# Kernel tuning notes

Hardware: AMD Instinct MI355X
Metric: run time of the kernel (lower is better)

The kernel has to match this reference:

```python
import jax, jax.numpy as jnp
import numpy as np

B, S, D, H = 4, 2048, 1024, 16


def setup_inputs() -> dict:
    key = jax.random.key(0)
    ks = jax.random.split(key, 9)
    scale = 0.02  # keep logits in a sane range
    x = jax.random.normal(ks[0], (B, S, D), dtype=jnp.float32)
    Wq = jax.random.normal(ks[1], (D, D), dtype=jnp.float32) * scale
    bq = jax.random.normal(ks[2], (D,), dtype=jnp.float32) * scale
    Wk = jax.random.normal(ks[3], (D, D), dtype=jnp.float32) * scale
    bk = jax.random.normal(ks[4], (D,), dtype=jnp.float32) * scale
    Wv = jax.random.normal(ks[5], (D, D), dtype=jnp.float32) * scale
    bv = jax.random.normal(ks[6], (D,), dtype=jnp.float32) * scale
    Wo = jax.random.normal(ks[7], (D, D), dtype=jnp.float32) * scale
    bo = jax.random.normal(ks[8], (D,), dtype=jnp.float32) * scale
    return {"x": x, "Wq": Wq, "bq": bq, "Wk": Wk, "bk": bk,
            "Wv": Wv, "bv": bv, "Wo": Wo, "bo": bo}


def _apply_rope(x):
    """Rotate-half RoPE over the full feature dim (applied pre-projection)."""
    b, s, d = x.shape
    half = d // 2
    # theta_i = 10000^(-2i/d), i in [0, d/2)
    freq = jnp.exp(jnp.arange(0, d, 2, dtype=jnp.float32) * (-np.log(10000.0) / d))
    ang = jnp.arange(s, dtype=jnp.float32)[:, None] * freq[None, :]  # [S, d/2]
    cos, sin = jnp.cos(ang), jnp.sin(ang)
    x1, x2 = x[..., :half], x[..., half:]
    return jnp.concatenate([x1 * cos - x2 * sin, x1 * sin + x2 * cos], axis=-1)


def reference(x, Wq, bq, Wk, bk, Wv, bv, Wo, bo):
    b, s, d = x.shape
    h = H
    hd = d // h
    rx = _apply_rope(x)  # [B, S, D]

    def proj(W, bias):
        y = rx @ W.T + bias                       # torch Linear: x W^T + b
        return y.reshape(b, s, h, hd).transpose(0, 2, 1, 3)  # [B, H, S, hd]

    q, k, v = proj(Wq, bq), proj(Wk, bk), proj(Wv, bv)
    scores = jnp.einsum('bhqd,bhkd->bhqk', q, k) / np.sqrt(hd)
    attn = jax.nn.softmax(scores, axis=-1)
    attended = jnp.einsum('bhqk,bhkd->bhqd', attn, v)
    attended = attended.transpose(0, 2, 1, 3).reshape(b, s, d)
    return attended @ Wo.T + bo
```

## Files before the change

kernel.cpp:

```cpp
#include <hip/hip_runtime.h>

#define NB 4
#define NS 2048
#define ND 1024
#define NH 16
#define HD 64

using bf16x8 = __attribute__((ext_vector_type(8))) short;
using f32x4  = __attribute__((ext_vector_type(4))) float;

__device__ __forceinline__ unsigned short f2bf(float f) {
  union { float f; unsigned u; } a; a.f = f;
  unsigned r = a.u + 0x7FFF + ((a.u >> 16) & 1);
  return (unsigned short)(r >> 16);
}

__device__ __forceinline__ void gload_lds16(const void* g, void* l) {
  __builtin_amdgcn_global_load_lds(
      (const __attribute__((address_space(1))) void*)g,
      (__attribute__((address_space(3))) void*)l, 16, 0, 0);
}

__global__ __launch_bounds__(256) void rope_kernel(const float* __restrict__ x,
                                                   unsigned short* __restrict__ rx) {
  int idx = blockIdx.x * 256 + threadIdx.x;
  int j  = idx & 511;
  int bs = idx >> 9;
  int s  = bs & (NS - 1);
  const float* xp = x + (size_t)bs * ND;
  float ang = (float)s * __expf((float)j * -0.017988946039f);
  float sn, cs;
  __sincosf(ang, &sn, &cs);
  float x1 = xp[j], x2 = xp[j + 512];
  unsigned short* rp = rx + (size_t)bs * ND;
  rp[j]       = f2bf(x1 * cs - x2 * sn);
  rp[j + 512] = f2bf(x1 * sn + x2 * cs);
}

__global__ __launch_bounds__(256) void wconv_kernel(const float* __restrict__ w0,
                                                    const float* __restrict__ w1,
                                                    const float* __restrict__ w2,
                                                    const float* __restrict__ w3,
                                                    unsigned short* __restrict__ wb) {
  int idx = blockIdx.x * 256 + threadIdx.x;
  int e = idx << 2;
  const float* w = (e < (1 << 20)) ? w0 : (e < (2 << 20)) ? w1 : (e < (3 << 20)) ? w2 : w3;
  float4 v = *(const float4*)(w + (e & 0xFFFFF));
  ushort4 o;
  o.x = f2bf(v.x); o.y = f2bf(v.y); o.z = f2bf(v.z); o.w = f2bf(v.w);
  *(ushort4*)(wb + e) = o;
}

__global__ __launch_bounds__(256) void gemm_qkv(const unsigned short* __restrict__ A,
                                                const unsigned short* __restrict__ Wb,
                                                const float* __restrict__ bq,
                                                const float* __restrict__ bk,
                                                const float* __restrict__ bv,
                                                unsigned short* __restrict__ q,
                                                unsigned short* __restrict__ k,
                                                unsigned short* __restrict__ vt) {
  __shared__ alignas(16) unsigned short As[128 * 32];
  __shared__ alignas(16) unsigned short Bs[128 * 32];
  const int tid = threadIdx.x;
  const int lane = tid & 63;
  const int wid = tid >> 6;
  const int wm = wid >> 1, wn = wid & 1;
  const int l15 = lane & 15, lg = lane >> 4;
  const int m0 = blockIdx.x * 128;
  const int n0 = blockIdx.y * 128;
  const int z = blockIdx.z;
  const unsigned short* Bp = Wb + ((size_t)z << 20);

  f32x4 acc[4][4] = {};

  for (int k0 = 0; k0 < ND; k0 += 32) {
#pragma unroll
    for (int it = 0; it < 2; ++it) {
      int c = it * 256 + tid;
      int row = c >> 2, kc = (c & 3) << 3;
      int ldsbase = (it * 256 + (tid & 192)) << 3;
      gload_lds16(A  + (size_t)(m0 + row) * ND + k0 + kc, As + ldsbase);
      gload_lds16(Bp + (size_t)(n0 + row) * ND + k0 + kc, Bs + ldsbase);
    }
    __syncthreads();
    bf16x8 af[4], bfr[4];
#pragma unroll
    for (int m = 0; m < 4; ++m)
      af[m] = *(const bf16x8*)(As + (wm * 64 + m * 16 + l15) * 32 + lg * 8);
#pragma unroll
    for (int n = 0; n < 4; ++n)
      bfr[n] = *(const bf16x8*)(Bs + (wn * 64 + n * 16 + l15) * 32 + lg * 8);
#pragma unroll
    for (int m = 0; m < 4; ++m)
#pragma unroll
      for (int n = 0; n < 4; ++n)
        acc[m][n] = __builtin_amdgcn_mfma_f32_16x16x32_bf16(af[m], bfr[n], acc[m][n], 0, 0, 0);
    __syncthreads();
  }

  const float* bias = (z == 0) ? bq : (z == 1) ? bk : bv;
#pragma unroll
  for (int n = 0; n < 4; ++n) {
    int col = n0 + wn * 64 + n * 16 + l15;
    float bb = bias[col];
    int hh = col >> 6, dd = col & 63;
#pragma unroll
    for (int m = 0; m < 4; ++m) {
#pragma unroll
      for (int r = 0; r < 4; ++r) {
        int rowi = m0 + wm * 64 + m * 16 + lg * 4 + r;
        int bbi = rowi >> 11, ss = rowi & (NS - 1);
        unsigned short val = f2bf(acc[m][n][r] + bb);
        size_t bhoff = (size_t)(bbi * NH + hh);
        if (z == 0)      q [(bhoff * NS + ss) * HD + dd] = val;
        else if (z == 1) k [(bhoff * NS + ss) * HD + dd] = val;
        else             vt[(bhoff * HD + dd) * NS + ss] = val;
      }
    }
  }
}

__global__ __launch_bounds__(256) void attn_kernel(const unsigned short* __restrict__ q,
                                                   const unsigned short* __restrict__ k,
                                                   const unsigned short* __restrict__ vt,
                                                   unsigned short* __restrict__ att) {
  __shared__ alignas(16) unsigned short Ks[2][64 * 64];
  __shared__ alignas(16) unsigned short Vs[2][64 * 64];
  __shared__ alignas(16) unsigned short Ps[4][32 * 64];
  const int tid = threadIdx.x;
  const int lane = tid & 63;
  const int w = tid >> 6;
  const int l15 = lane & 15, lg = lane >> 4;

  const int id = blockIdx.x;
  const int swz = (id & 7) * 128 + (id >> 3);
  const int bh = swz >> 4;
  const int b = bh >> 4, h = bh & 15;
  const int q0 = (swz & 15) * 128;

  const unsigned short* qp = q  + (size_t)bh * NS * HD;
  const unsigned short* kp = k  + (size_t)bh * NS * HD;
  const unsigned short* vp = vt + (size_t)bh * HD * NS;

  bf16x8 qf[2][2];
#pragma unroll
  for (int m = 0; m < 2; ++m)
#pragma unroll
    for (int t = 0; t < 2; ++t)
      qf[m][t] = *(const bf16x8*)(qp + (size_t)(q0 + w * 32 + m * 16 + l15) * HD + t * 32 + lg * 8);

  f32x4 o[2][4] = {};
  float run_m[2][4], run_l[2][4];
#pragma unroll
  for (int m = 0; m < 2; ++m)
#pragma unroll
    for (int r = 0; r < 4; ++r) { run_m[m][r] = -1e30f; run_l[m][r] = 0.f; }

  unsigned short* ps = &Ps[w][0];

  const int c0 = tid;
#define STAGE(buf, t0)                                                          \
  {                                                                             \
    _Pragma("unroll")                                                           \
    for (int it = 0; it < 2; ++it) {                                            \
      int c = it * 256 + c0;                                                    \
      int ro = c >> 3;                                                          \
      int chs = (c & 7) ^ (ro & 7);                                             \
      int ldsbase = (it * 256 + (tid & 192)) << 3;                              \
      gload_lds16(kp + (size_t)((t0) + ro) * HD + (chs << 3), Ks[buf] + ldsbase); \
      gload_lds16(vp + (size_t)ro * NS + (t0) + (chs << 3),   Vs[buf] + ldsbase); \
    }                                                                           \
  }

  STAGE(0, 0);
  __syncthreads();
  int cur = 0;

  for (int t0 = 0; t0 < NS; t0 += 64) {
    if (t0 + 64 < NS) STAGE(cur ^ 1, t0 + 64);

    f32x4 sc[2][4] = {};
#pragma unroll
    for (int kk = 0; kk < 2; ++kk)
#pragma unroll
      for (int n = 0; n < 4; ++n) {
        int krow = n * 16 + l15;
        bf16x8 kf = *(const bf16x8*)(Ks[cur] + krow * 64 + (((kk * 4 + lg) ^ (krow & 7)) << 3));
#pragma unroll
        for (int m = 0; m < 2; ++m)
          sc[m][n] = __builtin_amdgcn_mfma_f32_16x16x32_bf16(qf[m][kk], kf, sc[m][n], 0, 0, 0);
      }

#pragma unroll
    for (int m = 0; m < 2; ++m)
#pragma unroll
      for (int r = 0; r < 4; ++r) {
        float mx = fmaxf(fmaxf(sc[m][0][r], sc[m][1][r]), fmaxf(sc[m][2][r], sc[m][3][r]));
        mx = fmaxf(mx, __shfl_xor(mx, 1));
        mx = fmaxf(mx, __shfl_xor(mx, 2));
        mx = fmaxf(mx, __shfl_xor(mx, 4));
        mx = fmaxf(mx, __shfl_xor(mx, 8));
        float nm = fmaxf(run_m[m][r], mx);
        float fac = __expf(0.125f * (run_m[m][r] - nm));
        run_m[m][r] = nm;
        float rs = 0.f;
#pragma unroll
        for (int n = 0; n < 4; ++n) {
          float p = __expf(0.125f * (sc[m][n][r] - nm));
          sc[m][n][r] = p;
          rs += p;
        }
        rs += __shfl_xor(rs, 1);
        rs += __shfl_xor(rs, 2);
        rs += __shfl_xor(rs, 4);
        rs += __shfl_xor(rs, 8);
        run_l[m][r] = run_l[m][r] * fac + rs;
#pragma unroll
        for (int n = 0; n < 4; ++n) o[m][n][r] *= fac;
      }

#pragma unroll
    for (int m = 0; m < 2; ++m)
#pragma unroll
      for (int n = 0; n < 4; ++n)
#pragma unroll
        for (int r = 0; r < 4; ++r) {
          int prow = m * 16 + lg * 4 + r;
          ps[prow * 64 + ((n * 16 + l15) ^ ((prow & 7) << 3))] = f2bf(sc[m][n][r]);
        }

    bf16x8 pf[2][2];
#pragma unroll
    for (int m = 0; m < 2; ++m)
#pragma unroll
      for (int kk = 0; kk < 2; ++kk)
        pf[m][kk] = *(const bf16x8*)(ps + (m * 16 + l15) * 64 + (((kk * 4 + lg) ^ (l15 & 7)) << 3));

#pragma unroll
    for (int kk = 0; kk < 2; ++kk)
#pragma unroll
      for (int n = 0; n < 4; ++n) {
        int vrow = n * 16 + l15;
        bf16x8 vf = *(const bf16x8*)(Vs[cur] + vrow * 64 + (((kk * 4 + lg) ^ (vrow & 7)) << 3));
#pragma unroll
        for (int m = 0; m < 2; ++m)
          o[m][n] = __builtin_amdgcn_mfma_f32_16x16x32_bf16(pf[m][kk], vf, o[m][n], 0, 0, 0);
      }
    __syncthreads();
    cur ^= 1;
  }
#undef STAGE

#pragma unroll
  for (int m = 0; m < 2; ++m)
#pragma unroll
    for (int r = 0; r < 4; ++r) {
      int rowi = q0 + w * 32 + m * 16 + lg * 4 + r;
      float inv = 1.0f / run_l[m][r];
#pragma unroll
      for (int n = 0; n < 4; ++n)
        att[((size_t)(b * NS + rowi)) * ND + h * HD + n * 16 + l15] = f2bf(o[m][n][r] * inv);
    }
}

__global__ __launch_bounds__(256) void gemm_out(const unsigned short* __restrict__ A,
                                                const unsigned short* __restrict__ Bw,
                                                const float* __restrict__ bo,
                                                float* __restrict__ out) {
  __shared__ alignas(16) unsigned short As[128 * 32];
  __shared__ alignas(16) unsigned short Bs[128 * 32];
  const int tid = threadIdx.x;
  const int lane = tid & 63;
  const int wid = tid >> 6;
  const int wm = wid >> 1, wn = wid & 1;
  const int l15 = lane & 15, lg = lane >> 4;
  const int m0 = blockIdx.x * 128;
  const int n0 = blockIdx.y * 128;

  f32x4 acc[4][4] = {};

  for (int k0 = 0; k0 < ND; k0 += 32) {
#pragma unroll
    for (int it = 0; it < 2; ++it) {
      int c = it * 256 + tid;
      int row = c >> 2, kc = (c & 3) << 3;
      int ldsbase = (it * 256 + (tid & 192)) << 3;
      gload_lds16(A  + (size_t)(m0 + row) * ND + k0 + kc, As + ldsbase);
      gload_lds16(Bw + (size_t)(n0 + row) * ND + k0 + kc, Bs + ldsbase);
    }
    __syncthreads();
    bf16x8 af[4], bfr[4];
#pragma unroll
    for (int m = 0; m < 4; ++m)
      af[m] = *(const bf16x8*)(As + (wm * 64 + m * 16 + l15) * 32 + lg * 8);
#pragma unroll
    for (int n = 0; n < 4; ++n)
      bfr[n] = *(const bf16x8*)(Bs + (wn * 64 + n * 16 + l15) * 32 + lg * 8);
#pragma unroll
    for (int m = 0; m < 4; ++m)
#pragma unroll
      for (int n = 0; n < 4; ++n)
        acc[m][n] = __builtin_amdgcn_mfma_f32_16x16x32_bf16(af[m], bfr[n], acc[m][n], 0, 0, 0);
    __syncthreads();
  }

#pragma unroll
  for (int n = 0; n < 4; ++n) {
    int col = n0 + wn * 64 + n * 16 + l15;
    float bb = bo[col];
#pragma unroll
    for (int m = 0; m < 4; ++m)
#pragma unroll
      for (int r = 0; r < 4; ++r) {
        int rowi = m0 + wm * 64 + m * 16 + lg * 4 + r;
        out[(size_t)rowi * ND + col] = acc[m][n][r] + bb;
      }
  }
}

extern "C" void kernel_launch(void* const* d_in, const int* in_sizes, int n_in,
                              void* d_out, int out_size, void* d_ws, size_t ws_size,
                              hipStream_t stream) {
  const float* x  = (const float*)d_in[0];
  const float* Wq = (const float*)d_in[1];
  const float* bq = (const float*)d_in[2];
  const float* Wk = (const float*)d_in[3];
  const float* bk = (const float*)d_in[4];
  const float* Wv = (const float*)d_in[5];
  const float* bv = (const float*)d_in[6];
  const float* Wo = (const float*)d_in[7];
  const float* bo = (const float*)d_in[8];
  float* out = (float*)d_out;

  char* ws = (char*)d_ws;
  const size_t MB = 1024 * 1024;
  unsigned short* rx  = (unsigned short*)(ws);
  unsigned short* wb  = (unsigned short*)(ws + 16 * MB);
  unsigned short* qb  = (unsigned short*)(ws + 24 * MB);
  unsigned short* kb  = (unsigned short*)(ws + 40 * MB);
  unsigned short* vtb = (unsigned short*)(ws + 56 * MB);
  unsigned short* att = (unsigned short*)(ws + 72 * MB);

  rope_kernel<<<dim3(16384), dim3(256), 0, stream>>>(x, rx);
  wconv_kernel<<<dim3(4096), dim3(256), 0, stream>>>(Wq, Wk, Wv, Wo, wb);
  gemm_qkv<<<dim3(64, 8, 3), dim3(256), 0, stream>>>(rx, wb, bq, bk, bv, qb, kb, vtb);
  attn_kernel<<<dim3(1024), dim3(256), 0, stream>>>(qb, kb, vtb, att);
  gemm_out<<<dim3(64, 8), dim3(256), 0, stream>>>(att, wb + 3 * 1048576, bo, out);
}
```

Baseline: 427.9 us.

## Fold softmax scale into Q, use exp2, lazy rescale, shrink KV tile to 32

Q is pre-multiplied by log2(e)/sqrt(hd) in the projection epilogue so that attention can use the hardware v_exp_f32 (exp2) directly with no per-element scale multiply. The online softmax now rescales the output accumulator and running sum only when some row max rises by more than 4 (in log2 units) anywhere in the wavefront, which skips most rescale work. The KV tile shrinks from 64 to 32 keys, which halves LDS use and changes the swizzles and staging loads. In exchange, the loop runs twice as many iterations with twice as many barriers, and the deferred rescale lets exponents reach up to 2^4 before renormalising.

```diff
diff --git a/kernel.cpp b/kernel.cpp
--- a/kernel.cpp
+++ b/kernel.cpp
@@ -9,10 +9,18 @@
 using bf16x8 = __attribute__((ext_vector_type(8))) short;
 using f32x4  = __attribute__((ext_vector_type(4))) float;
 
+#define QSCALE 0.1803368801111804f
+
 __device__ __forceinline__ unsigned short f2bf(float f) {
   union { float f; unsigned u; } a; a.f = f;
   unsigned r = a.u + 0x7FFF + ((a.u >> 16) & 1);
   return (unsigned short)(r >> 16);
+}
+
+__device__ __forceinline__ float exp2_hw(float x) {
+  float r;
+  asm("v_exp_f32 %0, %1" : "=v"(r) : "v"(x));
+  return r;
 }
 
 __device__ __forceinline__ void gload_lds16(const void* g, void* l) {
@@ -110,7 +118,9 @@
       for (int r = 0; r < 4; ++r) {
         int rowi = m0 + wm * 64 + m * 16 + lg * 4 + r;
         int bbi = rowi >> 11, ss = rowi & (NS - 1);
-        unsigned short val = f2bf(acc[m][n][r] + bb);
+        float vv = acc[m][n][r] + bb;
+        if (z == 0) vv *= QSCALE;
+        unsigned short val = f2bf(vv);
         size_t bhoff = (size_t)(bbi * NH + hh);
         if (z == 0)      q [(bhoff * NS + ss) * HD + dd] = val;
         else if (z == 1) k [(bhoff * NS + ss) * HD + dd] = val;
@@ -124,9 +134,9 @@
                                                    const unsigned short* __restrict__ k,
                                                    const unsigned short* __restrict__ vt,
                                                    unsigned short* __restrict__ att) {
-  __shared__ alignas(16) unsigned short Ks[2][64 * 64];
-  __shared__ alignas(16) unsigned short Vs[2][64 * 64];
-  __shared__ alignas(16) unsigned short Ps[4][32 * 64];
+  __shared__ alignas(16) unsigned short Ks[2][32 * 64];
+  __shared__ alignas(16) unsigned short Vs[2][64 * 32];
+  __shared__ alignas(16) unsigned short Ps[4][32 * 32];
   const int tid = threadIdx.x;
   const int lane = tid & 63;
   const int w = tid >> 6;
@@ -157,33 +167,28 @@
     for (int r = 0; r < 4; ++r) { run_m[m][r] = -1e30f; run_l[m][r] = 0.f; }
 
   unsigned short* ps = &Ps[w][0];
-
-  const int c0 = tid;
-#define STAGE(buf, t0)                                                          \
-  {                                                                             \
-    _Pragma("unroll")                                                           \
-    for (int it = 0; it < 2; ++it) {                                            \
-      int c = it * 256 + c0;                                                    \
-      int ro = c >> 3;                                                          \
-      int chs = (c & 7) ^ (ro & 7);                                             \
-      int ldsbase = (it * 256 + (tid & 192)) << 3;                              \
-      gload_lds16(kp + (size_t)((t0) + ro) * HD + (chs << 3), Ks[buf] + ldsbase); \
-      gload_lds16(vp + (size_t)ro * NS + (t0) + (chs << 3),   Vs[buf] + ldsbase); \
-    }                                                                           \
+  const int ldsbase = (tid & 192) << 3;
+
+#define STAGE(buf, t0)                                                           \
+  {                                                                              \
+    int roK = tid >> 3, chK = (tid & 7) ^ (roK & 7);                             \
+    gload_lds16(kp + (size_t)((t0) + roK) * HD + (chK << 3), Ks[buf] + ldsbase); \
+    int roV = tid >> 2, chV = (tid & 3) ^ (roV & 3);                             \
+    gload_lds16(vp + (size_t)roV * NS + (t0) + (chV << 3),   Vs[buf] + ldsbase); \
   }
 
   STAGE(0, 0);
   __syncthreads();
   int cur = 0;
 
-  for (int t0 = 0; t0 < NS; t0 += 64) {
-    if (t0 + 64 < NS) STAGE(cur ^ 1, t0 + 64);
-
-    f32x4 sc[2][4] = {};
+  for (int t0 = 0; t0 < NS; t0 += 32) {
+    if (t0 + 32 < NS) STAGE(cur ^ 1, t0 + 32);
+
+    f32x4 sc[2][2] = {};
 #pragma unroll
     for (int kk = 0; kk < 2; ++kk)
 #pragma unroll
-      for (int n = 0; n < 4; ++n) {
+      for (int n = 0; n < 2; ++n) {
         int krow = n * 16 + l15;
         bf16x8 kf = *(const bf16x8*)(Ks[cur] + krow * 64 + (((kk * 4 + lg) ^ (krow & 7)) << 3));
 #pragma unroll
@@ -191,22 +196,42 @@
           sc[m][n] = __builtin_amdgcn_mfma_f32_16x16x32_bf16(qf[m][kk], kf, sc[m][n], 0, 0, 0);
       }
 
+    float mxv[2][4];
+    bool need = false;
 #pragma unroll
     for (int m = 0; m < 2; ++m)
 #pragma unroll
       for (int r = 0; r < 4; ++r) {
-        float mx = fmaxf(fmaxf(sc[m][0][r], sc[m][1][r]), fmaxf(sc[m][2][r], sc[m][3][r]));
+        float mx = fmaxf(sc[m][0][r], sc[m][1][r]);
         mx = fmaxf(mx, __shfl_xor(mx, 1));
         mx = fmaxf(mx, __shfl_xor(mx, 2));
         mx = fmaxf(mx, __shfl_xor(mx, 4));
         mx = fmaxf(mx, __shfl_xor(mx, 8));
-        float nm = fmaxf(run_m[m][r], mx);
-        float fac = __expf(0.125f * (run_m[m][r] - nm));
-        run_m[m][r] = nm;
+        mxv[m][r] = mx;
+        need = need || (mx > run_m[m][r] + 4.0f);
+      }
+    if (__any(need)) {
+#pragma unroll
+      for (int m = 0; m < 2; ++m)
+#pragma unroll
+        for (int r = 0; r < 4; ++r) {
+          float nm = fmaxf(run_m[m][r], mxv[m][r]);
+          float fac = exp2_hw(run_m[m][r] - nm);
+          run_m[m][r] = nm;
+          run_l[m][r] *= fac;
+#pragma unroll
+          for (int n = 0; n < 4; ++n) o[m][n][r] *= fac;
+        }
+    }
+
+#pragma unroll
+    for (int m = 0; m < 2; ++m)
+#pragma unroll
+      for (int r = 0; r < 4; ++r) {
         float rs = 0.f;
 #pragma unroll
-        for (int n = 0; n < 4; ++n) {
-          float p = __expf(0.125f * (sc[m][n][r] - nm));
+        for (int n = 0; n < 2; ++n) {
+          float p = exp2_hw(sc[m][n][r] - run_m[m][r]);
           sc[m][n][r] = p;
           rs += p;
         }
@@ -214,38 +239,35 @@
         rs += __shfl_xor(rs, 2);
         rs += __shfl_xor(rs, 4);
         rs += __shfl_xor(rs, 8);
-        run_l[m][r] = run_l[m][r] * fac + rs;
-#pragma unroll
-        for (int n = 0; n < 4; ++n) o[m][n][r] *= fac;
+        run_l[m][r] += rs;
       }
 
 #pragma unroll
     for (int m = 0; m < 2; ++m)
 #pragma unroll
-      for (int n = 0; n < 4; ++n)
+      for (int n = 0; n < 2; ++n)
 #pragma unroll
         for (int r = 0; r < 4; ++r) {
           int prow = m * 16 + lg * 4 + r;
-          ps[prow * 64 + ((n * 16 + l15) ^ ((prow & 7) << 3))] = f2bf(sc[m][n][r]);
+          int col = n * 16 + l15;
+          ps[prow * 32 + ((((col >> 3) ^ (prow & 3))) << 3) + (col & 7)] = f2bf(sc[m][n][r]);
         }
 
-    bf16x8 pf[2][2];
-#pragma unroll
-    for (int m = 0; m < 2; ++m)
-#pragma unroll
-      for (int kk = 0; kk < 2; ++kk)
-        pf[m][kk] = *(const bf16x8*)(ps + (m * 16 + l15) * 64 + (((kk * 4 + lg) ^ (l15 & 7)) << 3));
-
-#pragma unroll
-    for (int kk = 0; kk < 2; ++kk)
-#pragma unroll
-      for (int n = 0; n < 4; ++n) {
-        int vrow = n * 16 + l15;
-        bf16x8 vf = *(const bf16x8*)(Vs[cur] + vrow * 64 + (((kk * 4 + lg) ^ (vrow & 7)) << 3));
-#pragma unroll
-        for (int m = 0; m < 2; ++m)
-          o[m][n] = __builtin_amdgcn_mfma_f32_16x16x32_bf16(pf[m][kk], vf, o[m][n], 0, 0, 0);
-      }
+    bf16x8 pf[2];
+#pragma unroll
+    for (int m = 0; m < 2; ++m) {
+      int prow = m * 16 + l15;
+      pf[m] = *(const bf16x8*)(ps + prow * 32 + ((lg ^ (prow & 3)) << 3));
+    }
+
+#pragma unroll
+    for (int n = 0; n < 4; ++n) {
+      int vrow = n * 16 + l15;
+      bf16x8 vf = *(const bf16x8*)(Vs[cur] + vrow * 32 + ((lg ^ (vrow & 3)) << 3));
+#pragma unroll
+      for (int m = 0; m < 2; ++m)
+        o[m][n] = __builtin_amdgcn_mfma_f32_16x16x32_bf16(pf[m], vf, o[m][n], 0, 0, 0);
+    }
     __syncthreads();
     cur ^= 1;
   }
```

New measurement: 519.1 us. +21.3%, slower.

## Fold softmax scale into Q, use exp2, and skip rescale via lazy max

Applied to the files above, without the earlier changes.

Folds the 1/sqrt(hd)*log2(e) factor into Q at projection time so the attention loop can call the hardware exp2 instruction directly, without a multiply. It also adds a lazy online-softmax update: the running max and the output/denominator rescale only happen when some row's new max exceeds the running max by more than 4 (in log2 units), checked wave-wide with __any. This cuts per-tile exp and multiply work in the softmax stage. In exchange, unnormalized probabilities can reach up to 2^4, which adds a little range risk in bf16, and Q is now stored pre-scaled, which changes its rounding slightly.

```diff
diff --git a/kernel.cpp b/kernel.cpp
--- a/kernel.cpp
+++ b/kernel.cpp
@@ -9,10 +9,18 @@
 using bf16x8 = __attribute__((ext_vector_type(8))) short;
 using f32x4  = __attribute__((ext_vector_type(4))) float;
 
+#define QSCALE 0.1803368801111804f
+
 __device__ __forceinline__ unsigned short f2bf(float f) {
   union { float f; unsigned u; } a; a.f = f;
   unsigned r = a.u + 0x7FFF + ((a.u >> 16) & 1);
   return (unsigned short)(r >> 16);
+}
+
+__device__ __forceinline__ float exp2_hw(float x) {
+  float r;
+  asm("v_exp_f32 %0, %1" : "=v"(r) : "v"(x));
+  return r;
 }
 
 __device__ __forceinline__ void gload_lds16(const void* g, void* l) {
@@ -110,7 +118,9 @@
       for (int r = 0; r < 4; ++r) {
         int rowi = m0 + wm * 64 + m * 16 + lg * 4 + r;
         int bbi = rowi >> 11, ss = rowi & (NS - 1);
-        unsigned short val = f2bf(acc[m][n][r] + bb);
+        float vv = acc[m][n][r] + bb;
+        if (z == 0) vv *= QSCALE;
+        unsigned short val = f2bf(vv);
         size_t bhoff = (size_t)(bbi * NH + hh);
         if (z == 0)      q [(bhoff * NS + ss) * HD + dd] = val;
         else if (z == 1) k [(bhoff * NS + ss) * HD + dd] = val;
@@ -191,6 +201,8 @@
           sc[m][n] = __builtin_amdgcn_mfma_f32_16x16x32_bf16(qf[m][kk], kf, sc[m][n], 0, 0, 0);
       }
 
+    float mxv[2][4];
+    bool need = false;
 #pragma unroll
     for (int m = 0; m < 2; ++m)
 #pragma unroll
@@ -200,13 +212,31 @@
         mx = fmaxf(mx, __shfl_xor(mx, 2));
         mx = fmaxf(mx, __shfl_xor(mx, 4));
         mx = fmaxf(mx, __shfl_xor(mx, 8));
-        float nm = fmaxf(run_m[m][r], mx);
-        float fac = __expf(0.125f * (run_m[m][r] - nm));
-        run_m[m][r] = nm;
+        mxv[m][r] = mx;
+        need = need || (mx > run_m[m][r] + 4.0f);
+      }
+    if (__any(need)) {
+#pragma unroll
+      for (int m = 0; m < 2; ++m)
+#pragma unroll
+        for (int r = 0; r < 4; ++r) {
+          float nm = fmaxf(run_m[m][r], mxv[m][r]);
+          float fac = exp2_hw(run_m[m][r] - nm);
+          run_m[m][r] = nm;
+          run_l[m][r] *= fac;
+#pragma unroll
+          for (int n = 0; n < 4; ++n) o[m][n][r] *= fac;
+        }
+    }
+
+#pragma unroll
+    for (int m = 0; m < 2; ++m)
+#pragma unroll
+      for (int r = 0; r < 4; ++r) {
         float rs = 0.f;
 #pragma unroll
         for (int n = 0; n < 4; ++n) {
-          float p = __expf(0.125f * (sc[m][n][r] - nm));
+          float p = exp2_hw(sc[m][n][r] - run_m[m][r]);
           sc[m][n][r] = p;
           rs += p;
         }
@@ -214,9 +244,7 @@
         rs += __shfl_xor(rs, 2);
         rs += __shfl_xor(rs, 4);
         rs += __shfl_xor(rs, 8);
-        run_l[m][r] = run_l[m][r] * fac + rs;
-#pragma unroll
-        for (int n = 0; n < 4; ++n) o[m][n][r] *= fac;
+        run_l[m][r] += rs;
       }
 
 #pragma unroll
```

Measured after the change: 417.4 us. 1.03x faster.
